# Kernel tuning notes

Measured on AMD Instinct MI355X. Metric: run time of the kernel, lower is better.

Reference implementation:

```python
import jax, jax.numpy as jnp
import numpy as np
import math

NUM_BUCKETS = 32
MAX_DISTANCE = 128.0
LOG_BASE = 2.0


def relative_position_bucket(delta):
    # delta: float array. Mirrors torch version exactly.
    sign = jnp.sign(delta)
    n = jnp.clip(jnp.abs(delta), 1e-6, MAX_DISTANCE)
    log_index = jnp.floor(jnp.log(n) / math.log(LOG_BASE)).astype(jnp.int32)
    log_index = jnp.clip(log_index, 0, NUM_BUCKETS - 1)
    return log_index * sign.astype(jnp.int32) + (NUM_BUCKETS - 1)


def setup_inputs() -> dict:
    key = jax.random.key(0)
    ks = jax.random.split(key, 16)
    B, G, D, H = 4, 1024, 512, 8
    d_head = D // H
    inp = {
        "query": jax.random.normal(ks[0], (B, G, D), jnp.float32),
        "key": jax.random.normal(ks[1], (B, G, D), jnp.float32),
        "value": jax.random.normal(ks[2], (B, G, D), jnp.float32),
        # 2D coordinates spread over ~[-192, 192] so many log buckets are hit
        "coords": jax.random.normal(ks[3], (B, G, 2), jnp.float32) * 64.0,
        "mask": jax.random.randint(ks[4], (B, G), 0, 2, jnp.int32),
        # Linear params (torch convention: y = x @ W.T + b)
        "Wq": jax.random.normal(ks[5], (D, D), jnp.float32) / np.sqrt(D),
        "bq": jnp.zeros((D,), jnp.float32),
        "Wk": jax.random.normal(ks[6], (D, D), jnp.float32) / np.sqrt(D),
        "bk": jnp.zeros((D,), jnp.float32),
        "Wv": jax.random.normal(ks[7], (D, D), jnp.float32) / np.sqrt(D),
        "bv": jnp.zeros((D,), jnp.float32),
        "Wo": jax.random.normal(ks[8], (D, D), jnp.float32) / np.sqrt(D),
        "bo": jnp.zeros((D,), jnp.float32),
        # relative-position bias tables: (2*num_buckets - 1, num_heads)
        "rpe_x": jax.random.normal(ks[9], (2 * NUM_BUCKETS - 1, H), jnp.float32) * 0.02,
        "rpe_y": jax.random.normal(ks[10], (2 * NUM_BUCKETS - 1, H), jnp.float32) * 0.02,
    }
    return inp


def reference(query, key, value, coords, mask,
              Wq, bq, Wk, bk, Wv, bv, Wo, bo, rpe_x, rpe_y):
    B, Gq, D = query.shape
    Gk = key.shape[1]
    H = rpe_x.shape[1]
    d_head = D // H

    # projections -> (B, H, G, d_head)
    def proj(x, W, b, G):
        return (x @ W.T + b).reshape(B, G, H, d_head).transpose(0, 2, 1, 3)

    Q = proj(query, Wq, bq, Gq)
    K = proj(key, Wk, bk, Gk)
    V = proj(value, Wv, bv, Gk)

    scores = jnp.einsum('bhqd,bhkd->bhqk', Q, K) / math.sqrt(d_head)

    # relative-position bias from 2D coords
    delta = coords[:, :Gq, None, :] - coords[:, None, :Gk, :]  # (B, Gq, Gk, 2)
    bucket_x = relative_position_bucket(delta[..., 0])
    bucket_y = relative_position_bucket(delta[..., 1])
    rpe_bias = rpe_x[bucket_x] + rpe_y[bucket_y]               # (B, Gq, Gk, H)
    scores = scores + rpe_bias.transpose(0, 3, 1, 2)

    scores = jnp.where(mask[:, None, None, :] == 0, -jnp.inf, scores)
    attn = jax.nn.softmax(scores, axis=-1)
    out = jnp.einsum('bhqk,bhkd->bhqd', attn, V)
    out = out.transpose(0, 2, 1, 3).reshape(B, Gq, D)
    return out @ Wo.T + bo
```

## Files before the change

kernel.cpp:

```cpp
#include <hip/hip_runtime.h>
#include <hip/hip_bf16.h>

typedef __attribute__((ext_vector_type(8))) short bf16x8;
typedef __attribute__((ext_vector_type(4))) float f32x4;

__device__ __forceinline__ unsigned short f2bf(float x) {
  union { __hip_bfloat16 h; unsigned short u; } cv;
  cv.h = __float2bfloat16(x);
  return cv.u;
}

__device__ __forceinline__ void gload16(const void* g, void* l) {
  __builtin_amdgcn_global_load_lds(
      (const __attribute__((address_space(1))) unsigned int*)g,
      (__attribute__((address_space(3))) unsigned int*)l, 16, 0, 0);
}

__device__ __forceinline__ int swz128(int row, int colb) {
  return row * 128 + (colb ^ ((row & 7) << 4));
}

__global__ __launch_bounds__(256)
void k_cvt_all(const float* __restrict__ q, const float* __restrict__ k,
               const float* __restrict__ v, const float* __restrict__ Wq,
               const float* __restrict__ Wk, const float* __restrict__ Wv,
               const float* __restrict__ Wo,
               unsigned short* __restrict__ XQ, unsigned short* __restrict__ XK,
               unsigned short* __restrict__ XV, unsigned short* __restrict__ WQB,
               unsigned short* __restrict__ WKB, unsigned short* __restrict__ WVB,
               unsigned short* __restrict__ WOB)
{
  long i = ((long)blockIdx.x * 256 + threadIdx.x) * 8;
  const float* s; unsigned short* d; long off;
  if (i < 2097152)      { s = q; d = XQ; off = i; }
  else if (i < 4194304) { s = k; d = XK; off = i - 2097152; }
  else if (i < 6291456) { s = v; d = XV; off = i - 4194304; }
  else {
    long j = i - 6291456;
    int wsel = (int)(j >> 18);
    off = j & 262143;
    s = wsel == 0 ? Wq : wsel == 1 ? Wk : wsel == 2 ? Wv : Wo;
    d = wsel == 0 ? WQB : wsel == 1 ? WKB : wsel == 2 ? WVB : WOB;
  }
  float4 a = *(const float4*)(s + off);
  float4 bb = *(const float4*)(s + off + 4);
  bf16x8 o;
  o[0] = (short)f2bf(a.x);  o[1] = (short)f2bf(a.y);
  o[2] = (short)f2bf(a.z);  o[3] = (short)f2bf(a.w);
  o[4] = (short)f2bf(bb.x); o[5] = (short)f2bf(bb.y);
  o[6] = (short)f2bf(bb.z); o[7] = (short)f2bf(bb.w);
  *(bf16x8*)(d + off) = o;
}

__global__ __launch_bounds__(1024)
void k_scan(const int* __restrict__ mask, int* __restrict__ idx, int* __restrict__ cnt) {
  __shared__ int ps[1024];
  int b = blockIdx.x, t = threadIdx.x;
  int m = mask[(b << 10) + t];
  ps[t] = m;
  __syncthreads();
  #pragma unroll
  for (int off = 1; off < 1024; off <<= 1) {
    int v = (t >= off) ? ps[t - off] : 0;
    __syncthreads();
    ps[t] += v;
    __syncthreads();
  }
  if (m) idx[(b << 10) + ps[t] - 1] = t;
  if (t == 1023) cnt[b] = ps[t];
}

__device__ __forceinline__ int rbucket(float dd) {
  float ad = fabsf(dd);
  float n = fminf(fmaxf(ad, 1e-6f), 128.0f);
  int li = (int)floorf(logf(n) * 1.4426950408889634f);
  li = li < 0 ? 0 : (li > 31 ? 31 : li);
  int s = (dd > 0.f) ? 1 : ((dd < 0.f) ? -1 : 0);
  return li * s + 31;
}

__global__ __launch_bounds__(256)
void k_buckets_c(const float* __restrict__ coords, const int* __restrict__ idx,
                 const int* __restrict__ cnt, unsigned short* __restrict__ buk) {
  int b = blockIdx.y;
  int f = blockIdx.x * 256 + threadIdx.x;
  int qi = f >> 10, ck = f & 1023;
  if (ck >= cnt[b]) return;
  int ki = idx[(b << 10) + ck];
  const float* cb = coords + (b << 11);
  float dx = cb[qi * 2] - cb[ki * 2];
  float dy = cb[qi * 2 + 1] - cb[ki * 2 + 1];
  int bx = rbucket(dx);
  int by = rbucket(dy);
  buk[((long)(b << 10) + qi) * 1024 + ck] = (unsigned short)(bx | (by << 8));
}

__global__ __launch_bounds__(256)
void k_gatherKV(const unsigned short* __restrict__ KP,
                const unsigned short* __restrict__ VTMP,
                const int* __restrict__ idx, const int* __restrict__ cnt,
                unsigned short* __restrict__ KC, unsigned short* __restrict__ VCT)
{
  __shared__ unsigned short tile[64][68];
  __shared__ int lidx[64];
  int bh = blockIdx.y, b = bh >> 3;
  int cn = cnt[b];
  int ck0 = blockIdx.x << 6;
  if (ck0 >= cn) return;
  int t = threadIdx.x;
  if (t < 64) lidx[t] = idx[(b << 10) + min(ck0 + t, cn - 1)];
  __syncthreads();
  int r = t >> 2, qd = t & 3;
  long srcrow = ((long)(bh << 10) + lidx[r]) * 64;
  long dstrow = ((long)(bh << 10) + ck0 + r) * 64;
  uint4 kv0 = *(const uint4*)(KP + srcrow + qd * 16);
  uint4 kv1 = *(const uint4*)(KP + srcrow + qd * 16 + 8);
  *(uint4*)(KC + dstrow + qd * 16) = kv0;
  *(uint4*)(KC + dstrow + qd * 16 + 8) = kv1;
  const uint2* vsrc = (const uint2*)(VTMP + srcrow + qd * 16);
  #pragma unroll
  for (int s = 0; s < 4; ++s)
    *(uint2*)(&tile[r][qd * 16 + s * 4]) = vsrc[s];
  __syncthreads();
  #pragma unroll
  for (int it = 0; it < 16; ++it) {
    int d = it * 4 + (t >> 6);
    int ck = t & 63;
    VCT[((long)(bh << 6) + d) * 1024 + ck0 + ck] = tile[ck][d];
  }
}

__device__ __forceinline__ void gemm_core64(
    const unsigned short* __restrict__ A, const unsigned short* __restrict__ Bw,
    int m0, int n0, unsigned short* ldsA, unsigned short* ldsB, f32x4 acc[4][2])
{
  const int t = threadIdx.x;
  const int lane = t & 63;
  const int w = t >> 6;
  const int wm = (w >> 1) << 6;
  const int wn = (w & 1) << 5;
  const int l15 = lane & 15;
  const int l4 = lane >> 4;
  const f32x4 fz = {0.f, 0.f, 0.f, 0.f};

  #pragma unroll
  for (int r = 0; r < 4; ++r)
    #pragma unroll
    for (int c = 0; c < 2; ++c) acc[r][c] = fz;

  for (int k0 = 0; k0 < 512; k0 += 32) {
    #pragma unroll
    for (int rr = 0; rr < 2; ++rr) {
      int c = rr * 256 + t;
      int row = c >> 2, cc = c & 3;
      gload16(A + (m0 + row) * 512 + k0 + cc * 8, (char*)ldsA + c * 16);
    }
    {
      int c = t;
      int row = c >> 2, cc = c & 3;
      gload16(Bw + (n0 + row) * 512 + k0 + cc * 8, (char*)ldsB + c * 16);
    }
    __syncthreads();
    bf16x8 af[4], bfr[2];
    #pragma unroll
    for (int r = 0; r < 4; ++r)
      af[r] = *(const bf16x8*)((const char*)ldsA + (wm + r * 16 + l15) * 64 + l4 * 16);
    #pragma unroll
    for (int c = 0; c < 2; ++c)
      bfr[c] = *(const bf16x8*)((const char*)ldsB + (wn + c * 16 + l15) * 64 + l4 * 16);
    #pragma unroll
    for (int r = 0; r < 4; ++r)
      #pragma unroll
      for (int c = 0; c < 2; ++c)
        acc[r][c] = __builtin_amdgcn_mfma_f32_16x16x32_bf16(af[r], bfr[c], acc[r][c], 0, 0, 0);
    __syncthreads();
  }
}

__global__ __launch_bounds__(256)
void k_gemm_proj(const unsigned short* __restrict__ XQ, const unsigned short* __restrict__ XK,
                 const unsigned short* __restrict__ XV, const unsigned short* __restrict__ WQ,
                 const unsigned short* __restrict__ WK, const unsigned short* __restrict__ WV,
                 const float* __restrict__ bq, const float* __restrict__ bk,
                 const float* __restrict__ bv,
                 unsigned short* __restrict__ QP, unsigned short* __restrict__ KP,
                 unsigned short* __restrict__ VT)
{
  __shared__ unsigned short ldsA[128 * 32];
  __shared__ unsigned short ldsB[64 * 32];
  int z = blockIdx.z;
  const unsigned short* A = z == 0 ? XQ : z == 1 ? XK : XV;
  const unsigned short* W = z == 0 ? WQ : z == 1 ? WK : WV;
  const float* bias = z == 0 ? bq : z == 1 ? bk : bv;
  unsigned short* dst = z == 0 ? QP : z == 1 ? KP : VT;
  int m0 = blockIdx.x * 128, n0 = blockIdx.y * 64;
  f32x4 acc[4][2];
  gemm_core64(A, W, m0, n0, ldsA, ldsB, acc);

  const int t = threadIdx.x, lane = t & 63, w = t >> 6;
  const int wm = (w >> 1) << 6, wn = (w & 1) << 5;
  const int l15 = lane & 15, l4 = lane >> 4;
  #pragma unroll
  for (int r = 0; r < 4; ++r)
    #pragma unroll
    for (int c = 0; c < 2; ++c)
      #pragma unroll
      for (int i = 0; i < 4; ++i) {
        int m = m0 + wm + r * 16 + (l4 << 2) + i;
        int n = n0 + wn + c * 16 + l15;
        float y = acc[r][c][i] + bias[n];
        int b = m >> 10, g = m & 1023, hh = n >> 6, dd = n & 63;
        dst[((((b << 3) + hh) << 10) + g) * 64 + dd] = f2bf(y);
      }
}

__global__ __launch_bounds__(256)
void k_attn(const unsigned short* __restrict__ QP, const unsigned short* __restrict__ KC,
            const unsigned short* __restrict__ VCT, const unsigned short* __restrict__ BUKC,
            const int* __restrict__ cnt, const float* __restrict__ rpe_x,
            const float* __restrict__ rpe_y, unsigned short* __restrict__ AO)
{
  __shared__ float rx[64], ry[64];
  __shared__ unsigned short Ps[4][16 * 64];

  const int t = threadIdx.x;
  const int lane = t & 63;
  const int w = t >> 6;
  const int l15 = lane & 15;
  const int l4 = lane >> 4;
  const f32x4 fz = {0.f, 0.f, 0.f, 0.f};

  int g = blockIdx.x;
  int xcd = g & 7, slot = g >> 3;
  int b = xcd >> 1;
  int qb = ((xcd & 1) << 3) | (slot & 7);
  int h = slot >> 3;
  int bh = (b << 3) | h;
  int qw = (qb << 6) | (w << 4);

  if (t < 63) { rx[t] = rpe_x[t * 8 + h]; ry[t] = rpe_y[t * 8 + h]; }
  else if (t == 63) { rx[63] = 0.f; ry[63] = 0.f; }
  __syncthreads();

  const unsigned short* Qg = QP + ((long)(bh << 10) + qw) * 64;
  bf16x8 qf[2];
  #pragma unroll
  for (int ks = 0; ks < 2; ++ks)
    qf[ks] = *(const bf16x8*)(Qg + (long)l15 * 64 + ks * 32 + l4 * 8);

  const int cn = cnt[b];
  const int nkt = (cn + 63) >> 6;
  const unsigned short* Kg = KC + ((long)(bh << 10)) * 64;
  const unsigned short* Vg = VCT + ((long)(bh << 6)) * 1024;
  const unsigned short* bukb = BUKC + (((long)(b << 10) + qw) << 10);

  float mrun[4], lrun[4];
  f32x4 oacc[4];
  #pragma unroll
  for (int i = 0; i < 4; ++i) { mrun[i] = -1e30f; lrun[i] = 0.f; }
  #pragma unroll
  for (int dj = 0; dj < 4; ++dj) oacc[dj] = fz;

  unsigned short* Pw = &Ps[w][0];

  for (int kt = 0; kt < nkt; ++kt) {
    const int k0 = kt << 6;
    unsigned short bko[4][4];
    #pragma unroll
    for (int i = 0; i < 4; ++i)
      #pragma unroll
      for (int nj = 0; nj < 4; ++nj)
        bko[i][nj] = bukb[(((long)((l4 << 2) + i)) << 10) + k0 + nj * 16 + l15];

    f32x4 sacc[4];
    #pragma unroll
    for (int nj = 0; nj < 4; ++nj) sacc[nj] = fz;
    #pragma unroll
    for (int nj = 0; nj < 4; ++nj)
      #pragma unroll
      for (int ks = 0; ks < 2; ++ks) {
        bf16x8 kf = *(const bf16x8*)(Kg + (long)(k0 + nj * 16 + l15) * 64 + ks * 32 + l4 * 8);
        sacc[nj] = __builtin_amdgcn_mfma_f32_16x16x32_bf16(qf[ks], kf, sacc[nj], 0, 0, 0);
      }

    float fsc[4];
    float pv_[4][4];
    #pragma unroll
    for (int i = 0; i < 4; ++i) {
      float sv[4];
      float vm = -1e30f;
      #pragma unroll
      for (int nj = 0; nj < 4; ++nj) {
        unsigned bkv = bko[i][nj];
        float bias = rx[bkv & 63] + ry[(bkv >> 8) & 63];
        float s = fmaf(sacc[nj][i], 0.125f, bias);
        s = ((k0 + nj * 16 + l15) < cn) ? s : -1e30f;
        sv[nj] = s;
        vm = fmaxf(vm, s);
      }
      vm = fmaxf(vm, __shfl_xor(vm, 1));
      vm = fmaxf(vm, __shfl_xor(vm, 2));
      vm = fmaxf(vm, __shfl_xor(vm, 4));
      vm = fmaxf(vm, __shfl_xor(vm, 8));
      float mo = mrun[i];
      float mn = fmaxf(mo, vm);
      float f = __expf(mo - mn);
      float ps = 0.f;
      #pragma unroll
      for (int nj = 0; nj < 4; ++nj) {
        float p = __expf(sv[nj] - mn);
        pv_[i][nj] = p;
        ps += p;
      }
      ps += __shfl_xor(ps, 1);
      ps += __shfl_xor(ps, 2);
      ps += __shfl_xor(ps, 4);
      ps += __shfl_xor(ps, 8);
      lrun[i] = lrun[i] * f + ps;
      mrun[i] = mn;
      fsc[i] = f;
    }
    #pragma unroll
    for (int dj = 0; dj < 4; ++dj)
      #pragma unroll
      for (int i = 0; i < 4; ++i) oacc[dj][i] *= fsc[i];

    #pragma unroll
    for (int i = 0; i < 4; ++i) {
      int prow = (l4 << 2) + i;
      #pragma unroll
      for (int nj = 0; nj < 4; ++nj) {
        int pcolb = (nj * 16 + l15) * 2;
        *(unsigned short*)((char*)Pw + swz128(prow, pcolb)) = f2bf(pv_[i][nj]);
      }
    }
    bf16x8 pf[2];
    #pragma unroll
    for (int ks = 0; ks < 2; ++ks)
      pf[ks] = *(const bf16x8*)((const char*)Pw + swz128(l15, ks * 64 + l4 * 16));

    #pragma unroll
    for (int dj = 0; dj < 4; ++dj)
      #pragma unroll
      for (int ks = 0; ks < 2; ++ks) {
        bf16x8 vf = *(const bf16x8*)(Vg + (long)(dj * 16 + l15) * 1024 + k0 + ks * 32 + l4 * 8);
        oacc[dj] = __builtin_amdgcn_mfma_f32_16x16x32_bf16(pf[ks], vf, oacc[dj], 0, 0, 0);
      }
  }

  #pragma unroll
  for (int dj = 0; dj < 4; ++dj)
    #pragma unroll
    for (int i = 0; i < 4; ++i) {
      int gq = qw + (l4 << 2) + i;
      int dd = dj * 16 + l15;
      float o = oacc[dj][i] / lrun[i];
      AO[((long)((b << 10) + gq)) * 512 + h * 64 + dd] = f2bf(o);
    }
}

__global__ __launch_bounds__(256)
void k_gemm_out(const unsigned short* __restrict__ AO, const unsigned short* __restrict__ WO,
                const float* __restrict__ bo, float* __restrict__ out)
{
  __shared__ unsigned short ldsA[128 * 32];
  __shared__ unsigned short ldsB[64 * 32];
  int m0 = blockIdx.x * 128, n0 = blockIdx.y * 64;
  f32x4 acc[4][2];
  gemm_core64(AO, WO, m0, n0, ldsA, ldsB, acc);

  const int t = threadIdx.x, lane = t & 63, w = t >> 6;
  const int wm = (w >> 1) << 6, wn = (w & 1) << 5;
  const int l15 = lane & 15, l4 = lane >> 4;
  #pragma unroll
  for (int r = 0; r < 4; ++r)
    #pragma unroll
    for (int c = 0; c < 2; ++c)
      #pragma unroll
      for (int i = 0; i < 4; ++i) {
        int m = m0 + wm + r * 16 + (l4 << 2) + i;
        int n = n0 + wn + c * 16 + l15;
        out[(long)m * 512 + n] = acc[r][c][i] + bo[n];
      }
}

extern "C" void kernel_launch(void* const* d_in, const int* in_sizes, int n_in,
                              void* d_out, int out_size, void* d_ws, size_t ws_size,
                              hipStream_t stream) {
  const float* q      = (const float*)d_in[0];
  const float* k      = (const float*)d_in[1];
  const float* v      = (const float*)d_in[2];
  const float* coords = (const float*)d_in[3];
  const int*   mask   = (const int*)d_in[4];
  const float* Wq     = (const float*)d_in[5];
  const float* bq     = (const float*)d_in[6];
  const float* Wk     = (const float*)d_in[7];
  const float* bk     = (const float*)d_in[8];
  const float* Wv     = (const float*)d_in[9];
  const float* bv     = (const float*)d_in[10];
  const float* Wo     = (const float*)d_in[11];
  const float* bo     = (const float*)d_in[12];
  const float* rpe_x  = (const float*)d_in[13];
  const float* rpe_y  = (const float*)d_in[14];
  float* out = (float*)d_out;

  unsigned short* WQB  = (unsigned short*)d_ws;
  unsigned short* WKB  = WQB + 262144;
  unsigned short* WVB  = WKB + 262144;
  unsigned short* WOB  = WVB + 262144;
  unsigned short* XQ   = WOB + 262144;
  unsigned short* XK   = XQ + 2097152;
  unsigned short* XV   = XK + 2097152;
  unsigned short* QP   = XV + 2097152;
  unsigned short* KP   = QP + 2097152;
  unsigned short* VTMP = KP + 2097152;
  unsigned short* KC   = VTMP + 2097152;
  unsigned short* VCT  = KC + 2097152;
  unsigned short* AO   = VCT + 2097152;
  int* idxp            = (int*)(AO + 2097152);
  int* cntp            = idxp + 4096;
  unsigned short* BUKC = XQ;

  k_cvt_all<<<dim3(3584), dim3(256), 0, stream>>>(q, k, v, Wq, Wk, Wv, Wo,
                                                  XQ, XK, XV, WQB, WKB, WVB, WOB);
  k_scan<<<dim3(4), dim3(1024), 0, stream>>>(mask, idxp, cntp);
  k_gemm_proj<<<dim3(32, 8, 3), dim3(256), 0, stream>>>(XQ, XK, XV, WQB, WKB, WVB,
                                                        bq, bk, bv, QP, KP, VTMP);
  k_gatherKV<<<dim3(16, 32), dim3(256), 0, stream>>>(KP, VTMP, idxp, cntp, KC, VCT);
  k_buckets_c<<<dim3(4096, 4), dim3(256), 0, stream>>>(coords, idxp, cntp, BUKC);
  k_attn<<<dim3(512), dim3(256), 0, stream>>>(QP, KC, VCT, BUKC, cntp,
                                              rpe_x, rpe_y, AO);
  k_gemm_out<<<dim3(32, 8), dim3(256), 0, stream>>>(AO, WOB, bo, out);
}
```

Before: 181.0 us.

## Split attention key range across two wave groups and precombine RPE bias table

The attention kernel now runs 512 threads per block, with two groups of four waves each handling half of the key tiles. Their partial softmax states are merged through shared memory at the end using a flash-decoding style rescale. The bucket kernel writes a combined index (bx*63+by) into a permuted layout, and padded entries are zeroed. This lets each lane fetch its four bucket values with one 8-byte load and look up a precomputed 63x63 bias table instead of two separate tables. The intent is more parallelism per block and fewer scattered loads, at the cost of more LDS use and a merge step.

```diff
diff --git a/kernel.cpp b/kernel.cpp
--- a/kernel.cpp
+++ b/kernel.cpp
@@ -85,14 +85,19 @@
   int b = blockIdx.y;
   int f = blockIdx.x * 256 + threadIdx.x;
   int qi = f >> 10, ck = f & 1023;
-  if (ck >= cnt[b]) return;
-  int ki = idx[(b << 10) + ck];
-  const float* cb = coords + (b << 11);
-  float dx = cb[qi * 2] - cb[ki * 2];
-  float dy = cb[qi * 2 + 1] - cb[ki * 2 + 1];
-  int bx = rbucket(dx);
-  int by = rbucket(dy);
-  buk[((long)(b << 10) + qi) * 1024 + ck] = (unsigned short)(bx | (by << 8));
+  int cn = cnt[b];
+  int cnp = (cn + 63) & ~63;
+  if (ck >= cnp) return;
+  int pos = (ck & ~63) | ((ck & 15) << 2) | ((ck >> 4) & 3);
+  unsigned short val = 0;
+  if (ck < cn) {
+    int ki = idx[(b << 10) + ck];
+    const float* cb = coords + (b << 11);
+    float dx = cb[qi * 2]     - cb[ki * 2];
+    float dy = cb[qi * 2 + 1] - cb[ki * 2 + 1];
+    val = (unsigned short)(rbucket(dx) * 63 + rbucket(dy));
+  }
+  buk[((long)(b << 10) + qi) * 1024 + pos] = val;
 }
 
 __global__ __launch_bounds__(256)
@@ -214,18 +219,23 @@
       }
 }
 
-__global__ __launch_bounds__(256)
+__global__ __launch_bounds__(512, 4)
 void k_attn(const unsigned short* __restrict__ QP, const unsigned short* __restrict__ KC,
             const unsigned short* __restrict__ VCT, const unsigned short* __restrict__ BUKC,
             const int* __restrict__ cnt, const float* __restrict__ rpe_x,
             const float* __restrict__ rpe_y, unsigned short* __restrict__ AO)
 {
-  __shared__ float rx[64], ry[64];
-  __shared__ unsigned short Ps[4][16 * 64];
+  __shared__ float biasT[3969];
+  __shared__ unsigned short Ps[8][1024];
+  __shared__ float O2[4][16][68];
+  __shared__ float M2[4][16];
+  __shared__ float L2s[4][16];
 
   const int t = threadIdx.x;
   const int lane = t & 63;
   const int w = t >> 6;
+  const int rg = w & 3;
+  const int kh = w >> 2;
   const int l15 = lane & 15;
   const int l4 = lane >> 4;
   const f32x4 fz = {0.f, 0.f, 0.f, 0.f};
@@ -236,10 +246,12 @@
   int qb = ((xcd & 1) << 3) | (slot & 7);
   int h = slot >> 3;
   int bh = (b << 3) | h;
-  int qw = (qb << 6) | (w << 4);
-
-  if (t < 63) { rx[t] = rpe_x[t * 8 + h]; ry[t] = rpe_y[t * 8 + h]; }
-  else if (t == 63) { rx[63] = 0.f; ry[63] = 0.f; }
+  int qw = (qb << 6) | (rg << 4);
+
+  for (int j = t; j < 3969; j += 512) {
+    int bx = j / 63, by = j - bx * 63;
+    biasT[j] = rpe_x[bx * 8 + h] + rpe_y[by * 8 + h];
+  }
   __syncthreads();
 
   const unsigned short* Qg = QP + ((long)(bh << 10) + qw) * 64;
@@ -250,9 +262,12 @@
 
   const int cn = cnt[b];
   const int nkt = (cn + 63) >> 6;
+  const int nk0 = (nkt + 1) >> 1;
+  const int ktb = kh ? nk0 : 0;
+  const int kte = kh ? nkt : nk0;
   const unsigned short* Kg = KC + ((long)(bh << 10)) * 64;
   const unsigned short* Vg = VCT + ((long)(bh << 6)) * 1024;
-  const unsigned short* bukb = BUKC + (((long)(b << 10) + qw) << 10);
+  const unsigned short* bukb = BUKC + ((long)(b << 10) + qw) * 1024;
 
   float mrun[4], lrun[4];
   f32x4 oacc[4];
@@ -263,14 +278,18 @@
 
   unsigned short* Pw = &Ps[w][0];
 
-  for (int kt = 0; kt < nkt; ++kt) {
+  for (int kt = ktb; kt < kte; ++kt) {
     const int k0 = kt << 6;
-    unsigned short bko[4][4];
-    #pragma unroll
-    for (int i = 0; i < 4; ++i)
-      #pragma unroll
-      for (int nj = 0; nj < 4; ++nj)
-        bko[i][nj] = bukb[(((long)((l4 << 2) + i)) << 10) + k0 + nj * 16 + l15];
+    unsigned bko[4][4];
+    #pragma unroll
+    for (int i = 0; i < 4; ++i) {
+      uint2 bv = *(const uint2*)(bukb + ((l4 << 2) + i) * 1024 + k0 + (l15 << 2));
+      bko[i][0] = bv.x & 0xffff; bko[i][1] = bv.x >> 16;
+      bko[i][2] = bv.y & 0xffff; bko[i][3] = bv.y >> 16;
+    }
+    int vmask[4];
+    #pragma unroll
+    for (int nj = 0; nj < 4; ++nj) vmask[nj] = (k0 + nj * 16 + l15) < cn;
 
     f32x4 sacc[4];
     #pragma unroll
@@ -291,10 +310,9 @@
       float vm = -1e30f;
       #pragma unroll
       for (int nj = 0; nj < 4; ++nj) {
-        unsigned bkv = bko[i][nj];
-        float bias = rx[bkv & 63] + ry[(bkv >> 8) & 63];
+        float bias = biasT[bko[i][nj]];
         float s = fmaf(sacc[nj][i], 0.125f, bias);
-        s = ((k0 + nj * 16 + l15) < cn) ? s : -1e30f;
+        s = vmask[nj] ? s : -1e30f;
         sv[nj] = s;
         vm = fmaxf(vm, s);
       }
@@ -348,15 +366,45 @@
       }
   }
 
-  #pragma unroll
-  for (int dj = 0; dj < 4; ++dj)
+  if (w >= 4) {
+    #pragma unroll
+    for (int dj = 0; dj < 4; ++dj)
+      #pragma unroll
+      for (int i = 0; i < 4; ++i)
+        O2[w - 4][(l4 << 2) + i][dj * 16 + l15] = oacc[dj][i];
+    if (l15 == 0) {
+      #pragma unroll
+      for (int i = 0; i < 4; ++i) {
+        M2[w - 4][(l4 << 2) + i] = mrun[i];
+        L2s[w - 4][(l4 << 2) + i] = lrun[i];
+      }
+    }
+  }
+  __syncthreads();
+  if (w < 4) {
+    float fs1[4], fs2[4];
     #pragma unroll
     for (int i = 0; i < 4; ++i) {
-      int gq = qw + (l4 << 2) + i;
-      int dd = dj * 16 + l15;
-      float o = oacc[dj][i] / lrun[i];
-      AO[((long)((b << 10) + gq)) * 512 + h * 64 + dd] = f2bf(o);
-    }
+      int row = (l4 << 2) + i;
+      float m2 = M2[w][row], l2 = L2s[w][row];
+      float mn = fmaxf(mrun[i], m2);
+      float f1 = __expf(mrun[i] - mn);
+      float f2 = __expf(m2 - mn);
+      float linv = 1.f / (lrun[i] * f1 + l2 * f2);
+      fs1[i] = f1 * linv;
+      fs2[i] = f2 * linv;
+    }
+    #pragma unroll
+    for (int dj = 0; dj < 4; ++dj)
+      #pragma unroll
+      for (int i = 0; i < 4; ++i) {
+        int row = (l4 << 2) + i;
+        int gq = qw + row;
+        int dd = dj * 16 + l15;
+        float o = oacc[dj][i] * fs1[i] + O2[w][row][dd] * fs2[i];
+        AO[((long)((b << 10) + gq)) * 512 + h * 64 + dd] = f2bf(o);
+      }
+  }
 }
 
 __global__ __launch_bounds__(256)
@@ -428,7 +476,7 @@
                                                         bq, bk, bv, QP, KP, VTMP);
   k_gatherKV<<<dim3(16, 32), dim3(256), 0, stream>>>(KP, VTMP, idxp, cntp, KC, VCT);
   k_buckets_c<<<dim3(4096, 4), dim3(256), 0, stream>>>(coords, idxp, cntp, BUKC);
-  k_attn<<<dim3(512), dim3(256), 0, stream>>>(QP, KC, VCT, BUKC, cntp,
+  k_attn<<<dim3(512), dim3(512), 0, stream>>>(QP, KC, VCT, BUKC, cntp,
                                               rpe_x, rpe_y, AO);
   k_gemm_out<<<dim3(32, 8), dim3(256), 0, stream>>>(AO, WOB, bo, out);
 }
```

Result: no change. 182.2 us (+0.6%).
